# Optimization experiments

Hardware: AMD Instinct MI355X
Metric: run time of the kernel (lower is better)

Reference implementation:

```python
import jax, jax.numpy as jnp
import numpy as np

E = 500_000   # edges
N = 100_000   # nodes
Q = 256       # queries
N_REL = 200
R = 2 * N_REL + 1  # relation table rows (401)
D = 64        # in_dim
A = 64        # attn_dim
O = 64        # out_dim


def setup_inputs() -> dict:
    key = jax.random.key(0)
    ks = jax.random.split(key, 16)
    s = 1.0 / np.sqrt(D)
    # edges columns: [query_idx, head_ent, rel, tail_ent, sub_node, obj_node]
    col_q = jax.random.randint(ks[0], (E, 1), 0, Q)
    col_h = jax.random.randint(ks[1], (E, 1), 0, N)
    col_r = jax.random.randint(ks[2], (E, 1), 0, R)
    col_t = jax.random.randint(ks[3], (E, 1), 0, N)
    col_s = jax.random.randint(ks[4], (E, 1), 0, N)
    col_o = jax.random.randint(ks[5], (E, 1), 0, N)
    edges = jnp.concatenate([col_q, col_h, col_r, col_t, col_s, col_o], axis=1)
    return {
        "q_sub": jax.random.randint(ks[6], (Q,), 0, N),
        "q_emb": jax.random.normal(ks[7], (Q, D), dtype=jnp.float32),
        "rela_embed": jax.random.normal(ks[8], (R, D), dtype=jnp.float32),
        "hidden": jax.random.normal(ks[9], (N, D), dtype=jnp.float32),
        "edges": edges,
        "n_nodes": N,
        "Ws_W": jax.random.normal(ks[10], (A, D), dtype=jnp.float32) * s,
        "Ws_b": jnp.zeros((A,), dtype=jnp.float32),
        "Wr_W": jax.random.normal(ks[11], (A, D), dtype=jnp.float32) * s,
        "Wq_W": jax.random.normal(ks[12], (A, D), dtype=jnp.float32) * s,
        "Wqr_W": jax.random.normal(ks[13], (A, D), dtype=jnp.float32) * s,
        "wa_W": jax.random.normal(ks[14], (1, A), dtype=jnp.float32) * s,
        "wa_b": jnp.zeros((1,), dtype=jnp.float32),
        "Wh_W": jax.random.normal(ks[15], (O, D), dtype=jnp.float32) * s,
    }


def reference(q_sub, q_emb, rela_embed, hidden, edges, n_nodes,
              Ws_W, Ws_b, Wr_W, Wq_W, Wqr_W, wa_W, wa_b, Wh_W):
    # sample_flag == 0 path of GNNLayer.forward (use_lama_rel == 1, act = identity)
    sub = edges[:, 4]
    rel = edges[:, 2]
    obj = edges[:, 5]
    hs = hidden[sub]            # [E, D] gather
    hr = rela_embed[rel]        # [E, D] gather
    h_qr = q_emb[edges[:, 0]]   # [E, D] gather
    # attention MLP: sigmoid(w_alpha(ReLU(Ws hs + Wr hr + Wq hqr + Wqr (hr*hqr))))
    pre = (jnp.einsum('ed,ad->ea', hs, Ws_W) + Ws_b
           + jnp.einsum('ed,ad->ea', hr, Wr_W)
           + jnp.einsum('ed,ad->ea', h_qr, Wq_W)
           + jnp.einsum('ed,ad->ea', hr * h_qr, Wqr_W))
    alpha = jax.nn.sigmoid(jnp.einsum('ea,oa->eo', jax.nn.relu(pre), wa_W) + wa_b)  # [E,1]
    message = alpha * (hs * hr)                                # [E, D]
    message_agg = jax.ops.segment_sum(message, obj, num_segments=n_nodes)  # [N, D] scatter-sum
    hidden_new = jnp.einsum('nd,od->no', message_agg, Wh_W)    # act = identity
    return hidden_new, alpha
```

## Files before the change

kernel.cpp:

```cpp
#include <hip/hip_runtime.h>
#include <hip/hip_bf16.h>

#define EDGES  500000
#define NNODES 100000
#define QN     256
#define RN     401
#define DD     64
#define AA     64
#define OO     64
#define XSB    1563
#define PB     1604
#define EB     15625

typedef __attribute__((ext_vector_type(8))) short short8;
typedef __attribute__((ext_vector_type(2))) short short2v;
typedef __attribute__((ext_vector_type(4))) float f32x4;
typedef __attribute__((ext_vector_type(2))) float f32x2;

__device__ inline unsigned short f2bf(float f) {
    union { float f; unsigned int u; } v; v.f = f;
    unsigned int u = v.u;
    u += 0x7FFFu + ((u >> 16) & 1u);
    return (unsigned short)(u >> 16);
}

__device__ inline unsigned pack2bf(float lo, float hi) {
    return (unsigned)f2bf(lo) | ((unsigned)f2bf(hi) << 16);
}

__device__ inline f32x2 bfpair2f(unsigned int u) {
    union { unsigned int i; float f; } lo, hi;
    lo.i = u << 16;
    hi.i = u & 0xFFFF0000u;
    f32x2 r; r[0] = lo.f; r[1] = hi.f; return r;
}

__device__ inline short8 load8_cvt(const float* __restrict__ p) {
    f32x4 x0 = ((const f32x4*)p)[0];
    f32x4 x1 = ((const f32x4*)p)[1];
    short8 r;
    r[0] = (short)f2bf(x0[0]); r[1] = (short)f2bf(x0[1]);
    r[2] = (short)f2bf(x0[2]); r[3] = (short)f2bf(x0[3]);
    r[4] = (short)f2bf(x1[0]); r[5] = (short)f2bf(x1[1]);
    r[6] = (short)f2bf(x1[2]); r[7] = (short)f2bf(x1[3]);
    return r;
}

__device__ inline short8 load8_cvt_prod(const float* __restrict__ pa,
                                        const float* __restrict__ pb) {
    f32x4 a0 = ((const f32x4*)pa)[0];
    f32x4 a1 = ((const f32x4*)pa)[1];
    f32x4 b0 = ((const f32x4*)pb)[0];
    f32x4 b1 = ((const f32x4*)pb)[1];
    short8 r;
    r[0] = (short)f2bf(a0[0]*b0[0]); r[1] = (short)f2bf(a0[1]*b0[1]);
    r[2] = (short)f2bf(a0[2]*b0[2]); r[3] = (short)f2bf(a0[3]*b0[3]);
    r[4] = (short)f2bf(a1[0]*b1[0]); r[5] = (short)f2bf(a1[1]*b1[1]);
    r[6] = (short)f2bf(a1[2]*b1[2]); r[7] = (short)f2bf(a1[3]*b1[3]);
    return r;
}

__device__ inline void atomic_pk_add_bf16(short* addr, short2v v) {
#if __has_builtin(__builtin_amdgcn_global_atomic_fadd_v2bf16)
    __builtin_amdgcn_global_atomic_fadd_v2bf16(
        (__attribute__((address_space(1))) short2v*)addr, v);
#else
    asm volatile("global_atomic_pk_add_bf16 %0, %1, off"
                 :: "v"(addr), "v"(v) : "memory");
#endif
}

__device__ inline void atomic_pk_add_bf16_u(short* addr, unsigned v) {
    atomic_pk_add_bf16(addr, __builtin_bit_cast(short2v, v));
}

struct Params {
    const float* hidden; const float* Ws_W; const float* q_emb; const float* rela;
    const float* Wq_W;   const float* Wr_W; const float* Wqr_W; const float* Ws_b;
    const int*   edges;  const float* wa_W; const float* wa_b;  const float* Wh_W;
    short* Xs; short* hidden_bf; short* P; short* agg;
    float* out; float* alpha_out;
};

__global__ void k_pre(Params pr) {
    __shared__ short W[AA * 200];
    __shared__ short stage[4][16 * 72];
    int tid = threadIdx.x;
    int wave = tid >> 6, lane = tid & 63;
    int quad = lane >> 4, l15 = lane & 15;
    short* st = stage[wave];

    if (blockIdx.x < XSB) {
        int rowbase_blk = blockIdx.x * 64;
        {
            const short8 z = short8{0,0,0,0,0,0,0,0};
            int base = rowbase_blk * DD + tid * 16;
            int row0 = rowbase_blk + (tid >> 2);
            if (row0 < NNODES) {
                *(short8*)(pr.agg + base) = z;
                *(short8*)(pr.agg + base + 8) = z;
            }
        }
        for (int idx = tid; idx < (AA * DD) / 2; idx += 256) {
            int a = idx >> 5, d2 = (idx & 31) * 2;
            f32x2 x = *(const f32x2*)(pr.Ws_W + a * 64 + d2);
            *reinterpret_cast<unsigned*>(&W[a * 72 + d2]) = pack2bf(x[0], x[1]);
        }
        __syncthreads();
        int rowbase = rowbase_blk + wave * 16;
        int row_a = rowbase + l15;
        f32x4 acc[4];
        for (int t = 0; t < 4; ++t) { acc[t][0]=acc[t][1]=acc[t][2]=acc[t][3]=0.f; }
#pragma unroll
        for (int ks = 0; ks < 2; ++ks) {
            int ka = ks * 32 + quad * 8;
            short8 afrag;
            if (row_a < NNODES) {
                afrag = load8_cvt(pr.hidden + (size_t)row_a * DD + ka);
                *(short8*)(pr.hidden_bf + (size_t)row_a * DD + ka) = afrag;
            } else {
                afrag = short8{0,0,0,0,0,0,0,0};
            }
#pragma unroll
            for (int t = 0; t < 4; ++t) {
                short8 bfrag = *(const short8*)&W[(t * 16 + l15) * 72 + ka];
                acc[t] = __builtin_amdgcn_mfma_f32_16x16x32_bf16(afrag, bfrag, acc[t], 0, 0, 0);
            }
        }
#pragma unroll
        for (int t = 0; t < 4; ++t)
#pragma unroll
            for (int r = 0; r < 4; ++r)
                st[(quad * 4 + r) * 72 + t * 16 + l15] = (short)f2bf(acc[t][r]);
        asm volatile("s_waitcnt lgkmcnt(0)" ::: "memory");
#pragma unroll
        for (int i = 0; i < 2; ++i) {
            int rr = i * 8 + (lane >> 3);
            int cc = (lane & 7) * 8;
            int grow = rowbase + rr;
            if (grow < NNODES) {
                short8 v = *(short8*)&st[rr * 72 + cc];
                *(short8*)&pr.Xs[(size_t)grow * AA + cc] = v;
            }
        }
    } else {
        int pb = blockIdx.x - XSB;
#pragma unroll
        for (int m = 0; m < 3; ++m) {
            const float* src = (m == 0) ? pr.Wq_W : (m == 1) ? pr.Wr_W : pr.Wqr_W;
            for (int idx = tid; idx < (AA * DD) / 2; idx += 256) {
                int a = idx >> 5, d2 = (idx & 31) * 2;
                f32x2 x = *(const f32x2*)(src + a * 64 + d2);
                *reinterpret_cast<unsigned*>(&W[a * 200 + m * 64 + d2]) =
                    pack2bf(x[0], x[1]);
            }
        }
        __syncthreads();
        int pairbase = pb * 64 + wave * 16;
        int mypair = pairbase + l15;
        int q = mypair / RN;
        int r = mypair - q * RN;
        const float* hq = pr.q_emb + (size_t)q * DD;
        const float* hr = pr.rela  + (size_t)r * DD;
        f32x4 acc[4];
#pragma unroll
        for (int t = 0; t < 4; ++t) {
            float b = pr.Ws_b[t * 16 + l15];
            acc[t][0] = acc[t][1] = acc[t][2] = acc[t][3] = b;
        }
#pragma unroll
        for (int ks = 0; ks < 6; ++ks) {
            int ka = ks * 32 + quad * 8;
            short8 afrag;
            if (ka < 64)       afrag = load8_cvt(hq + ka);
            else if (ka < 128) afrag = load8_cvt(hr + (ka - 64));
            else               afrag = load8_cvt_prod(hq + (ka - 128), hr + (ka - 128));
#pragma unroll
            for (int t = 0; t < 4; ++t) {
                short8 bfrag = *(const short8*)&W[(t * 16 + l15) * 200 + ka];
                acc[t] = __builtin_amdgcn_mfma_f32_16x16x32_bf16(afrag, bfrag, acc[t], 0, 0, 0);
            }
        }
#pragma unroll
        for (int t = 0; t < 4; ++t)
#pragma unroll
            for (int rg = 0; rg < 4; ++rg)
                st[(quad * 4 + rg) * 72 + t * 16 + l15] = (short)f2bf(acc[t][rg]);
        asm volatile("s_waitcnt lgkmcnt(0)" ::: "memory");
#pragma unroll
        for (int i = 0; i < 2; ++i) {
            int rr = i * 8 + (lane >> 3);
            int cc = (lane & 7) * 8;
            int prow = pairbase + rr;
            short8 v = *(short8*)&st[rr * 72 + cc];
            *(short8*)&pr.P[(size_t)prow * AA + cc] = v;
        }
    }
}

__global__ void k_edge(Params pr) {
    int tid  = threadIdx.x;
    int lane = tid & 63;
    int l8   = tid & 7;
    int g    = lane >> 3;
    int wave = tid >> 6;
    size_t ewave = (size_t)blockIdx.x * 32 + wave * 8;
    size_t e = ewave + g;

    const int* ebase = pr.edges + ewave * 6;
    int eval = (lane < 48) ? ebase[lane] : 0;
    int q   = __shfl(eval, g * 6 + 0, 64);
    int r   = __shfl(eval, g * 6 + 2, 64);
    int sub = __shfl(eval, g * 6 + 4, 64);
    int qr  = q * RN + r;
    int c8  = l8 * 8;

    short8 xs8 = *(const short8*)(pr.Xs + (size_t)sub * AA + c8);
    short8 pp8 = *(const short8*)(pr.P  + (size_t)qr  * AA + c8);
    f32x4 waA = *(const f32x4*)(pr.wa_W + c8);
    f32x4 waB = *(const f32x4*)(pr.wa_W + c8 + 4);

    typedef __attribute__((ext_vector_type(4))) unsigned int uint4v;
    uint4v xu = __builtin_bit_cast(uint4v, xs8);
    uint4v pu = __builtin_bit_cast(uint4v, pp8);
    f32x2 acc2; acc2[0] = 0.f; acc2[1] = 0.f;
#pragma unroll
    for (int j = 0; j < 4; ++j) {
        f32x2 a = bfpair2f(xu[j]);
        f32x2 b = bfpair2f(pu[j]);
        f32x2 s = a + b;
        float wlo = (j < 2) ? waA[2*j]     : waB[2*j - 4];
        float whi = (j < 2) ? waA[2*j + 1] : waB[2*j - 3];
        acc2[0] += fmaxf(s[0], 0.f) * wlo;
        acc2[1] += fmaxf(s[1], 0.f) * whi;
    }
    float v = acc2[0] + acc2[1];
    v += __shfl_xor(v, 1, 64);
    v += __shfl_xor(v, 2, 64);
    v += __shfl_xor(v, 4, 64);
    float alpha = 1.f / (1.f + __expf(-(v + pr.wa_b[0])));
    if (l8 == 0) pr.alpha_out[e] = alpha;

    int half = lane >> 5;
    int c2   = (lane & 31) * 2;
#pragma unroll
    for (int pass = 0; pass < 4; ++pass) {
        int ge    = pass * 2 + half;
        int sub_p = __shfl(eval, ge * 6 + 4, 64);
        int r_p   = __shfl(eval, ge * 6 + 2, 64);
        int obj_p = __shfl(eval, ge * 6 + 5, 64);
        float al  = __shfl(alpha, ge * 8, 64);
        unsigned hs_u = *(const unsigned*)&pr.hidden_bf[(size_t)sub_p * DD + c2];
        f32x2 hs = bfpair2f(hs_u);
        f32x2 hr = *(const f32x2*)&pr.rela[(size_t)r_p * DD + c2];
        atomic_pk_add_bf16_u(pr.agg + (size_t)obj_p * DD + c2,
                             pack2bf(al * hs[0] * hr[0], al * hs[1] * hr[1]));
    }
}

__global__ void k_out(Params pr) {
    __shared__ short W[OO * 72];
    __shared__ float stF[4][16 * 68];
    int tid = threadIdx.x;
    for (int idx = tid; idx < (OO * DD) / 2; idx += 256) {
        int o = idx >> 5, d2 = (idx & 31) * 2;
        f32x2 x = *(const f32x2*)(pr.Wh_W + o * 64 + d2);
        *reinterpret_cast<unsigned*>(&W[o * 72 + d2]) = pack2bf(x[0], x[1]);
    }
    __syncthreads();
    int wave = tid >> 6, lane = tid & 63;
    int quad = lane >> 4, l15 = lane & 15;
    int rowbase = blockIdx.x * 64 + wave * 16;
    int row_a = rowbase + l15;
    float* st = stF[wave];

    f32x4 acc[4];
    for (int t = 0; t < 4; ++t) { acc[t][0]=acc[t][1]=acc[t][2]=acc[t][3]=0.f; }
#pragma unroll
    for (int ks = 0; ks < 2; ++ks) {
        int ka = ks * 32 + quad * 8;
        short8 afrag;
        if (row_a < NNODES) afrag = *(const short8*)(pr.agg + (size_t)row_a * DD + ka);
        else                afrag = short8{0,0,0,0,0,0,0,0};
#pragma unroll
        for (int t = 0; t < 4; ++t) {
            short8 bfrag = *(const short8*)&W[(t * 16 + l15) * 72 + ka];
            acc[t] = __builtin_amdgcn_mfma_f32_16x16x32_bf16(afrag, bfrag, acc[t], 0, 0, 0);
        }
    }
#pragma unroll
    for (int t = 0; t < 4; ++t)
#pragma unroll
        for (int r = 0; r < 4; ++r)
            st[(quad * 4 + r) * 68 + t * 16 + l15] = acc[t][r];
    asm volatile("s_waitcnt lgkmcnt(0)" ::: "memory");
#pragma unroll
    for (int i = 0; i < 4; ++i) {
        int rr = i * 4 + (lane >> 4);
        int cc = (lane & 15) * 4;
        int grow = rowbase + rr;
        if (grow < NNODES) {
            f32x4 v = *(f32x4*)&st[rr * 68 + cc];
            *(f32x4*)&pr.out[(size_t)grow * OO + cc] = v;
        }
    }
}

extern "C" void kernel_launch(void* const* d_in, const int* in_sizes, int n_in,
                              void* d_out, int out_size, void* d_ws, size_t ws_size,
                              hipStream_t stream) {
    Params pr;
    pr.q_emb  = (const float*)d_in[1];
    pr.rela   = (const float*)d_in[2];
    pr.hidden = (const float*)d_in[3];
    pr.edges  = (const int*)d_in[4];
    pr.Ws_W   = (const float*)d_in[6];
    pr.Ws_b   = (const float*)d_in[7];
    pr.Wr_W   = (const float*)d_in[8];
    pr.Wq_W   = (const float*)d_in[9];
    pr.Wqr_W  = (const float*)d_in[10];
    pr.wa_W   = (const float*)d_in[11];
    pr.wa_b   = (const float*)d_in[12];
    pr.Wh_W   = (const float*)d_in[13];

    short* Xs        = (short*)d_ws;
    short* P         = Xs + (size_t)NNODES * AA;
    short* hidden_bf = P + (size_t)QN * RN * AA;
    short* agg       = hidden_bf + (size_t)NNODES * DD;
    pr.Xs = Xs; pr.P = P; pr.hidden_bf = hidden_bf; pr.agg = agg;

    pr.out       = (float*)d_out;
    pr.alpha_out = pr.out + (size_t)NNODES * OO;

    k_pre<<<XSB + PB, 256, 0, stream>>>(pr);
    k_edge<<<EB, 256, 0, stream>>>(pr);
    k_out<<<XSB, 256, 0, stream>>>(pr);
}
```

Measured before the change: 197.2 us.

## Split precompute into a bf16 table-conversion kernel plus separate Xs and P GEMM kernels

Adds a conversion kernel that turns hidden, q_emb, rela_embed and all weight matrices into bf16 tables once, and zeroes the aggregation buffer. The Xs and P projection kernels then read these bf16 tables directly instead of converting fp32 and rebuilding shared-memory weight tiles in every block. This removes redundant per-block weight conversion and halves the input bytes read by the GEMMs. In exchange it adds two kernel launches and an extra write-and-read pass over hidden, and it keeps scratch tables in the output buffer, which is safe only if the later kernels overwrite that region.

```diff
diff --git a/kernel.cpp b/kernel.cpp
--- a/kernel.cpp
+++ b/kernel.cpp
@@ -11,11 +11,18 @@
 #define XSB    1563
 #define PB     1604
 #define EB     15625
+#define TB_H   3125
+#define TB_Q   8
+#define TB_R   13
+#define TB_W3  6
+#define TB_WS  2
+#define TABB   (TB_H + TB_Q + TB_R + TB_W3 + TB_WS)
 
 typedef __attribute__((ext_vector_type(8))) short short8;
 typedef __attribute__((ext_vector_type(2))) short short2v;
 typedef __attribute__((ext_vector_type(4))) float f32x4;
 typedef __attribute__((ext_vector_type(2))) float f32x2;
+typedef __attribute__((ext_vector_type(4))) unsigned int uint4v;
 
 __device__ inline unsigned short f2bf(float f) {
     union { float f; unsigned int u; } v; v.f = f;
@@ -46,18 +53,20 @@
     return r;
 }
 
-__device__ inline short8 load8_cvt_prod(const float* __restrict__ pa,
-                                        const float* __restrict__ pb) {
-    f32x4 a0 = ((const f32x4*)pa)[0];
-    f32x4 a1 = ((const f32x4*)pa)[1];
-    f32x4 b0 = ((const f32x4*)pb)[0];
-    f32x4 b1 = ((const f32x4*)pb)[1];
-    short8 r;
-    r[0] = (short)f2bf(a0[0]*b0[0]); r[1] = (short)f2bf(a0[1]*b0[1]);
-    r[2] = (short)f2bf(a0[2]*b0[2]); r[3] = (short)f2bf(a0[3]*b0[3]);
-    r[4] = (short)f2bf(a1[0]*b1[0]); r[5] = (short)f2bf(a1[1]*b1[1]);
-    r[6] = (short)f2bf(a1[2]*b1[2]); r[7] = (short)f2bf(a1[3]*b1[3]);
-    return r;
+__device__ inline short8 prod8_bf(const short* __restrict__ pa,
+                                  const short* __restrict__ pb) {
+    short8 a = *(const short8*)pa;
+    short8 b = *(const short8*)pb;
+    uint4v au = __builtin_bit_cast(uint4v, a);
+    uint4v bu = __builtin_bit_cast(uint4v, b);
+    uint4v ru;
+#pragma unroll
+    for (int j = 0; j < 4; ++j) {
+        f32x2 x = bfpair2f(au[j]);
+        f32x2 y = bfpair2f(bu[j]);
+        ru[j] = pack2bf(x[0] * y[0], x[1] * y[1]);
+    }
+    return __builtin_bit_cast(short8, ru);
 }
 
 __device__ inline void atomic_pk_add_bf16(short* addr, short2v v) {
@@ -79,122 +88,124 @@
     const float* Wq_W;   const float* Wr_W; const float* Wqr_W; const float* Ws_b;
     const int*   edges;  const float* wa_W; const float* wa_b;  const float* Wh_W;
     short* Xs; short* hidden_bf; short* P; short* agg;
+    short* q_bf; short* r_bf; short* w3_bf; short* ws_bf;
     float* out; float* alpha_out;
 };
 
-__global__ void k_pre(Params pr) {
-    __shared__ short W[AA * 200];
+__global__ void k_tab(Params pr) {
+    int tid = threadIdx.x;
+    int b = blockIdx.x;
+    if (b < TB_H) {
+        size_t idx = (size_t)b * 2048 + tid * 8;
+        short8 v = load8_cvt(pr.hidden + idx);
+        *(short8*)(pr.hidden_bf + idx) = v;
+        *(short8*)(pr.agg + idx) = short8{0,0,0,0,0,0,0,0};
+    } else if (b < TB_H + TB_Q) {
+        int idx = (b - TB_H) * 2048 + tid * 8;
+        *(short8*)(pr.q_bf + idx) = load8_cvt(pr.q_emb + idx);
+    } else if (b < TB_H + TB_Q + TB_R) {
+        int idx = (b - TB_H - TB_Q) * 2048 + tid * 8;
+        if (idx < RN * DD)
+            *(short8*)(pr.r_bf + idx) = load8_cvt(pr.rela + idx);
+    } else if (b < TB_H + TB_Q + TB_R + TB_W3) {
+        int idx = (b - TB_H - TB_Q - TB_R) * 2048 + tid * 8;
+        int a = idx / 192, k = idx - a * 192;
+        const float* src = (k < 64)  ? pr.Wq_W  + a * 64 + k
+                         : (k < 128) ? pr.Wr_W  + a * 64 + (k - 64)
+                                     : pr.Wqr_W + a * 64 + (k - 128);
+        *(short8*)(pr.w3_bf + idx) = load8_cvt(src);
+    } else {
+        int idx = (b - TB_H - TB_Q - TB_R - TB_W3) * 2048 + tid * 8;
+        *(short8*)(pr.ws_bf + idx) = load8_cvt(pr.Ws_W + idx);
+    }
+}
+
+__global__ void k_xs(Params pr) {
     __shared__ short stage[4][16 * 72];
     int tid = threadIdx.x;
     int wave = tid >> 6, lane = tid & 63;
     int quad = lane >> 4, l15 = lane & 15;
     short* st = stage[wave];
 
-    if (blockIdx.x < XSB) {
-        int rowbase_blk = blockIdx.x * 64;
-        {
-            const short8 z = short8{0,0,0,0,0,0,0,0};
-            int base = rowbase_blk * DD + tid * 16;
-            int row0 = rowbase_blk + (tid >> 2);
-            if (row0 < NNODES) {
-                *(short8*)(pr.agg + base) = z;
-                *(short8*)(pr.agg + base + 8) = z;
-            }
-        }
-        for (int idx = tid; idx < (AA * DD) / 2; idx += 256) {
-            int a = idx >> 5, d2 = (idx & 31) * 2;
-            f32x2 x = *(const f32x2*)(pr.Ws_W + a * 64 + d2);
-            *reinterpret_cast<unsigned*>(&W[a * 72 + d2]) = pack2bf(x[0], x[1]);
-        }
-        __syncthreads();
-        int rowbase = rowbase_blk + wave * 16;
-        int row_a = rowbase + l15;
-        f32x4 acc[4];
-        for (int t = 0; t < 4; ++t) { acc[t][0]=acc[t][1]=acc[t][2]=acc[t][3]=0.f; }
-#pragma unroll
-        for (int ks = 0; ks < 2; ++ks) {
-            int ka = ks * 32 + quad * 8;
-            short8 afrag;
-            if (row_a < NNODES) {
-                afrag = load8_cvt(pr.hidden + (size_t)row_a * DD + ka);
-                *(short8*)(pr.hidden_bf + (size_t)row_a * DD + ka) = afrag;
-            } else {
-                afrag = short8{0,0,0,0,0,0,0,0};
-            }
-#pragma unroll
-            for (int t = 0; t < 4; ++t) {
-                short8 bfrag = *(const short8*)&W[(t * 16 + l15) * 72 + ka];
-                acc[t] = __builtin_amdgcn_mfma_f32_16x16x32_bf16(afrag, bfrag, acc[t], 0, 0, 0);
-            }
-        }
-#pragma unroll
-        for (int t = 0; t < 4; ++t)
-#pragma unroll
-            for (int r = 0; r < 4; ++r)
-                st[(quad * 4 + r) * 72 + t * 16 + l15] = (short)f2bf(acc[t][r]);
-        asm volatile("s_waitcnt lgkmcnt(0)" ::: "memory");
-#pragma unroll
-        for (int i = 0; i < 2; ++i) {
-            int rr = i * 8 + (lane >> 3);
-            int cc = (lane & 7) * 8;
-            int grow = rowbase + rr;
-            if (grow < NNODES) {
-                short8 v = *(short8*)&st[rr * 72 + cc];
-                *(short8*)&pr.Xs[(size_t)grow * AA + cc] = v;
-            }
-        }
-    } else {
-        int pb = blockIdx.x - XSB;
-#pragma unroll
-        for (int m = 0; m < 3; ++m) {
-            const float* src = (m == 0) ? pr.Wq_W : (m == 1) ? pr.Wr_W : pr.Wqr_W;
-            for (int idx = tid; idx < (AA * DD) / 2; idx += 256) {
-                int a = idx >> 5, d2 = (idx & 31) * 2;
-                f32x2 x = *(const f32x2*)(src + a * 64 + d2);
-                *reinterpret_cast<unsigned*>(&W[a * 200 + m * 64 + d2]) =
-                    pack2bf(x[0], x[1]);
-            }
-        }
-        __syncthreads();
-        int pairbase = pb * 64 + wave * 16;
-        int mypair = pairbase + l15;
-        int q = mypair / RN;
-        int r = mypair - q * RN;
-        const float* hq = pr.q_emb + (size_t)q * DD;
-        const float* hr = pr.rela  + (size_t)r * DD;
-        f32x4 acc[4];
+    int rowbase = blockIdx.x * 64 + wave * 16;
+    int row_a = rowbase + l15;
+    f32x4 acc[4];
+    for (int t = 0; t < 4; ++t) { acc[t][0]=acc[t][1]=acc[t][2]=acc[t][3]=0.f; }
+#pragma unroll
+    for (int ks = 0; ks < 2; ++ks) {
+        int ka = ks * 32 + quad * 8;
+        short8 afrag;
+        if (row_a < NNODES) afrag = *(const short8*)(pr.hidden_bf + (size_t)row_a * DD + ka);
+        else                afrag = short8{0,0,0,0,0,0,0,0};
 #pragma unroll
         for (int t = 0; t < 4; ++t) {
-            float b = pr.Ws_b[t * 16 + l15];
-            acc[t][0] = acc[t][1] = acc[t][2] = acc[t][3] = b;
-        }
-#pragma unroll
-        for (int ks = 0; ks < 6; ++ks) {
-            int ka = ks * 32 + quad * 8;
-            short8 afrag;
-            if (ka < 64)       afrag = load8_cvt(hq + ka);
-            else if (ka < 128) afrag = load8_cvt(hr + (ka - 64));
-            else               afrag = load8_cvt_prod(hq + (ka - 128), hr + (ka - 128));
-#pragma unroll
-            for (int t = 0; t < 4; ++t) {
-                short8 bfrag = *(const short8*)&W[(t * 16 + l15) * 200 + ka];
-                acc[t] = __builtin_amdgcn_mfma_f32_16x16x32_bf16(afrag, bfrag, acc[t], 0, 0, 0);
-            }
-        }
-#pragma unroll
-        for (int t = 0; t < 4; ++t)
-#pragma unroll
-            for (int rg = 0; rg < 4; ++rg)
-                st[(quad * 4 + rg) * 72 + t * 16 + l15] = (short)f2bf(acc[t][rg]);
-        asm volatile("s_waitcnt lgkmcnt(0)" ::: "memory");
-#pragma unroll
-        for (int i = 0; i < 2; ++i) {
-            int rr = i * 8 + (lane >> 3);
-            int cc = (lane & 7) * 8;
-            int prow = pairbase + rr;
+            short8 bfrag = *(const short8*)(pr.ws_bf + (t * 16 + l15) * DD + ka);
+            acc[t] = __builtin_amdgcn_mfma_f32_16x16x32_bf16(afrag, bfrag, acc[t], 0, 0, 0);
+        }
+    }
+#pragma unroll
+    for (int t = 0; t < 4; ++t)
+#pragma unroll
+        for (int r = 0; r < 4; ++r)
+            st[(quad * 4 + r) * 72 + t * 16 + l15] = (short)f2bf(acc[t][r]);
+    asm volatile("s_waitcnt lgkmcnt(0)" ::: "memory");
+#pragma unroll
+    for (int i = 0; i < 2; ++i) {
+        int rr = i * 8 + (lane >> 3);
+        int cc = (lane & 7) * 8;
+        int grow = rowbase + rr;
+        if (grow < NNODES) {
             short8 v = *(short8*)&st[rr * 72 + cc];
-            *(short8*)&pr.P[(size_t)prow * AA + cc] = v;
-        }
+            *(short8*)&pr.Xs[(size_t)grow * AA + cc] = v;
+        }
+    }
+}
+
+__global__ void k_p(Params pr) {
+    __shared__ short stage[4][16 * 72];
+    int tid = threadIdx.x;
+    int wave = tid >> 6, lane = tid & 63;
+    int quad = lane >> 4, l15 = lane & 15;
+    short* st = stage[wave];
+
+    int pairbase = blockIdx.x * 64 + wave * 16;
+    int mypair = pairbase + l15;
+    int q = mypair / RN;
+    int r = mypair - q * RN;
+    const short* hqb = pr.q_bf + (size_t)q * DD;
+    const short* hrb = pr.r_bf + (size_t)r * DD;
+    f32x4 acc[4];
+#pragma unroll
+    for (int t = 0; t < 4; ++t) {
+        float b = pr.Ws_b[t * 16 + l15];
+        acc[t][0] = acc[t][1] = acc[t][2] = acc[t][3] = b;
+    }
+#pragma unroll
+    for (int ks = 0; ks < 6; ++ks) {
+        int ka = ks * 32 + quad * 8;
+        short8 afrag;
+        if (ka < 64)       afrag = *(const short8*)(hqb + ka);
+        else if (ka < 128) afrag = *(const short8*)(hrb + (ka - 64));
+        else               afrag = prod8_bf(hqb + (ka - 128), hrb + (ka - 128));
+#pragma unroll
+        for (int t = 0; t < 4; ++t) {
+            short8 bfrag = *(const short8*)(pr.w3_bf + (t * 16 + l15) * 192 + ka);
+            acc[t] = __builtin_amdgcn_mfma_f32_16x16x32_bf16(afrag, bfrag, acc[t], 0, 0, 0);
+        }
+    }
+#pragma unroll
+    for (int t = 0; t < 4; ++t)
+#pragma unroll
+        for (int rg = 0; rg < 4; ++rg)
+            st[(quad * 4 + rg) * 72 + t * 16 + l15] = (short)f2bf(acc[t][rg]);
+    asm volatile("s_waitcnt lgkmcnt(0)" ::: "memory");
+#pragma unroll
+    for (int i = 0; i < 2; ++i) {
+        int rr = i * 8 + (lane >> 3);
+        int cc = (lane & 7) * 8;
+        int prow = pairbase + rr;
+        short8 v = *(short8*)&st[rr * 72 + cc];
+        *(short8*)&pr.P[(size_t)prow * AA + cc] = v;
     }
 }
 
@@ -220,7 +231,6 @@
     f32x4 waA = *(const f32x4*)(pr.wa_W + c8);
     f32x4 waB = *(const f32x4*)(pr.wa_W + c8 + 4);
 
-    typedef __attribute__((ext_vector_type(4))) unsigned int uint4v;
     uint4v xu = __builtin_bit_cast(uint4v, xs8);
     uint4v pu = __builtin_bit_cast(uint4v, pp8);
     f32x2 acc2; acc2[0] = 0.f; acc2[1] = 0.f;
@@ -332,7 +342,15 @@
     pr.out       = (float*)d_out;
     pr.alpha_out = pr.out + (size_t)NNODES * OO;
 
-    k_pre<<<XSB + PB, 256, 0, stream>>>(pr);
-    k_edge<<<EB, 256, 0, stream>>>(pr);
-    k_out<<<XSB, 256, 0, stream>>>(pr);
-}
+    short* scr = (short*)d_out;
+    pr.q_bf  = scr;
+    pr.r_bf  = pr.q_bf  + QN * DD;
+    pr.w3_bf = pr.r_bf  + RN * DD;
+    pr.ws_bf = pr.w3_bf + AA * 192;
+
+    k_tab<<<TABB, 256, 0, stream>>>(pr);
+    k_xs <<<XSB,  256, 0, stream>>>(pr);
+    k_p  <<<PB,   256, 0, stream>>>(pr);
+    k_edge<<<EB,  256, 0, stream>>>(pr);
+    k_out<<<XSB,  256, 0, stream>>>(pr);
+}
```

Result: slower. 213.2 us (+8.1%).
